# Optimization experiments

Hardware: AMD Instinct MI355X
Metric: run time of the kernel (lower is better)

## Reference

```python
import jax, jax.numpy as jnp
import numpy as np

HEADS = 16
DIM_HEAD = 64
NEG_INF = -1e30


def _rope_cos_sin(seq_len, dim_head, dtype):
    inv_freq = 1.0 / (10000.0 ** (jnp.arange(0, dim_head, 2, dtype=jnp.float32) / dim_head))
    t = jnp.arange(seq_len, dtype=jnp.float32)
    freqs = jnp.einsum('i,j->ij', t, inv_freq)          # [n, dh/2]
    emb = jnp.concatenate([freqs, freqs], axis=-1)       # [n, dh]
    return jnp.cos(emb).astype(dtype), jnp.sin(emb).astype(dtype)


def _rotate_half(x):
    x1, x2 = jnp.split(x, 2, axis=-1)
    return jnp.concatenate([-x2, x1], axis=-1)


def setup_inputs() -> dict:
    key = jax.random.key(0)
    k1, k2, k3 = jax.random.split(key, 3)
    dim = HEADS * DIM_HEAD  # 1024
    x = jax.random.normal(k1, (2, 2048, dim), dtype=jnp.float32)
    w_qkv = jax.random.normal(k2, (dim, 3 * dim), dtype=jnp.float32) * (dim ** -0.5)
    w_out = jax.random.normal(k3, (dim, dim), dtype=jnp.float32) * (dim ** -0.5)
    return {"x": x, "w_qkv": w_qkv, "w_out": w_out}


def reference(x, w_qkv, w_out):
    b, n, d = x.shape
    h, dh = HEADS, DIM_HEAD
    scale = dh ** -0.5

    qkv = x @ w_qkv                                      # [b, n, 3*h*dh]
    q, k, v = jnp.split(qkv, 3, axis=-1)
    reshape = lambda t: t.reshape(b, n, h, dh).transpose(0, 2, 1, 3)  # b h n dh
    q, k, v = reshape(q), reshape(k), reshape(v)

    cos, sin = _rope_cos_sin(n, dh, x.dtype)
    cos = cos[None, None, :, :]
    sin = sin[None, None, :, :]
    q = q * cos + _rotate_half(q) * sin
    k = k * cos + _rotate_half(k) * sin

    scores = jnp.einsum('bhid,bhjd->bhij', q, k) * scale  # [b, h, n, n]
    causal = jnp.triu(jnp.ones((n, n), dtype=bool), k=1)
    scores = jnp.where(causal[None, None, :, :], NEG_INF, scores)
    attn = jax.nn.softmax(scores, axis=-1)

    out = jnp.einsum('bhij,bhjd->bhid', attn, v)          # [b, h, n, dh]
    out = out.transpose(0, 2, 1, 3).reshape(b, n, h * dh)
    return out @ w_out
```

## Files before the change

### kernel.cpp

```cpp
#include <hip/hip_runtime.h>

#define SEQ 2048
#define NH 16
#define DH 64
#define DMODEL 1024
#define NQKV 3072

typedef __attribute__((ext_vector_type(8))) short bf16x8;
typedef __attribute__((ext_vector_type(4))) short bf16x4;
typedef __attribute__((ext_vector_type(4))) float f32x4;

#define GLOAD16(src, dst)                                                              \
  __builtin_amdgcn_global_load_lds((const __attribute__((address_space(1))) void*)(src), \
                                   (__attribute__((address_space(3))) void*)(dst), 16, 0, 0)

#define EXP2(x) __builtin_amdgcn_exp2f(x)

__device__ __forceinline__ unsigned short f2bf(float f) {
  union { float f; unsigned u; } v; v.f = f;
  unsigned r = v.u + 0x7FFFu + ((v.u >> 16) & 1u);
  return (unsigned short)(r >> 16);
}

__device__ __forceinline__ unsigned pkbf(float a, float b) {
  unsigned r;
  asm("v_cvt_pk_bf16_f32 %0, %1, %2" : "=v"(r) : "v"(a), "v"(b));
  return r;
}

__device__ __forceinline__ void transw_body(const float* __restrict__ in,
                                            unsigned short* __restrict__ out,
                                            int K, int N, int k0, int n0, int tid,
                                            float (*Ts)[65]) {
#pragma unroll
  for (int p = 0; p < 4; ++p) {
    int id = p * 256 + tid;
    int r = id >> 4, c4 = (id & 15) * 4;
    const f32x4 v = *reinterpret_cast<const f32x4*>(&in[(size_t)(k0 + r) * N + n0 + c4]);
    Ts[r][c4] = v[0]; Ts[r][c4 + 1] = v[1]; Ts[r][c4 + 2] = v[2]; Ts[r][c4 + 3] = v[3];
  }
  __syncthreads();
#pragma unroll
  for (int p = 0; p < 2; ++p) {
    int id = p * 256 + tid;
    int n = id >> 3, k8 = (id & 7) * 8;
    unsigned short tmp[8];
#pragma unroll
    for (int i = 0; i < 8; ++i) tmp[i] = f2bf(Ts[k8 + i][n]);
    *reinterpret_cast<bf16x8*>(&out[(size_t)(n0 + n) * K + k0 + k8]) =
        *reinterpret_cast<bf16x8*>(tmp);
  }
}

__global__ __launch_bounds__(256) void prep_kernel(
    const float* __restrict__ x, const float* __restrict__ w_qkv,
    const float* __restrict__ w_out, unsigned short* __restrict__ Xb,
    unsigned short* __restrict__ WqkvT, unsigned short* __restrict__ WoutT,
    float* __restrict__ cost, float* __restrict__ sint) {
  __shared__ float Ts[64][65];
  const int tid = threadIdx.x;
  const int id = blockIdx.x;
  if (id < 2048) {
    int idx = id * 256 + tid;
    const f32x4 v0 = *reinterpret_cast<const f32x4*>(&x[(size_t)idx * 8]);
    const f32x4 v1 = *reinterpret_cast<const f32x4*>(&x[(size_t)idx * 8 + 4]);
    bf16x8 o;
    o[0] = (short)f2bf(v0[0]); o[1] = (short)f2bf(v0[1]);
    o[2] = (short)f2bf(v0[2]); o[3] = (short)f2bf(v0[3]);
    o[4] = (short)f2bf(v1[0]); o[5] = (short)f2bf(v1[1]);
    o[6] = (short)f2bf(v1[2]); o[7] = (short)f2bf(v1[3]);
    *reinterpret_cast<bf16x8*>(&Xb[(size_t)idx * 8]) = o;
  } else if (id < 2816) {
    int t = id - 2048;
    transw_body(w_qkv, WqkvT, DMODEL, NQKV, (t & 15) * 64, (t >> 4) * 64, tid, Ts);
  } else if (id < 3072) {
    int t = id - 2816;
    transw_body(w_out, WoutT, DMODEL, DMODEL, (t & 15) * 64, (t >> 4) * 64, tid, Ts);
  } else {
    int idx = (id - 3072) * 256 + tid;
    int t = idx >> 5, j = idx & 31;
    float inv = powf(10000.0f, -(float)(2 * j) / 64.0f);
    float a = (float)t * inv;
    cost[idx] = cosf(a);
    sint[idx] = sinf(a);
  }
}

__global__ __launch_bounds__(256) void gemm_qkv_kernel(
    const unsigned short* __restrict__ Xb, const unsigned short* __restrict__ BT,
    unsigned short* __restrict__ Qb, unsigned short* __restrict__ Kb,
    unsigned short* __restrict__ Vtg,
    const float* __restrict__ cost, const float* __restrict__ sint) {
  __shared__ unsigned short As[2][8192];
  __shared__ unsigned short Bs[2][8192];

  const int tid = threadIdx.x;
  const int lane = tid & 63;
  const int w = tid >> 6;
  const int lam = lane & 15;
  const int g = lane >> 4;
  const int wr = w >> 1, wc = w & 1;
  const int rowBase = blockIdx.x * 128;
  const int colBase = blockIdx.y * 128;

  f32x4 acc[4][4];
#pragma unroll
  for (int m = 0; m < 4; ++m)
#pragma unroll
    for (int n = 0; n < 4; ++n) acc[m][n] = (f32x4){0.f, 0.f, 0.f, 0.f};

#define GSTAGE(buf, kk0)                                                               \
  {                                                                                    \
    _Pragma("unroll") for (int c = 0; c < 4; ++c) {                                    \
      int ch = c * 256 + w * 64 + lane;                                                \
      int row = ch >> 3, q = ch & 7;                                                   \
      GLOAD16(Xb + (size_t)(rowBase + row) * DMODEL + (kk0) + ((q ^ (row & 7)) * 8),   \
              &As[buf][0] + (c * 256 + w * 64) * 8);                                   \
      GLOAD16(BT + (size_t)(colBase + row) * DMODEL + (kk0) + ((q ^ (row & 7)) * 8),   \
              &Bs[buf][0] + (c * 256 + w * 64) * 8);                                   \
    }                                                                                  \
  }

  GSTAGE(0, 0);

  for (int kb = 0; kb < 16; ++kb) {
    if (kb + 1 < 16) {
      GSTAGE((kb + 1) & 1, (kb + 1) * 64);
      asm volatile("s_waitcnt vmcnt(8)" ::: "memory");
    } else {
      asm volatile("s_waitcnt vmcnt(0)" ::: "memory");
    }
    __builtin_amdgcn_s_barrier();
    const int cb = kb & 1;
#pragma unroll
    for (int kh = 0; kh < 2; ++kh) {
      bf16x8 a[4], b[4];
#pragma unroll
      for (int m = 0; m < 4; ++m) {
        int row = wr * 64 + m * 16 + lam;
        a[m] = *reinterpret_cast<bf16x8*>(&As[cb][row * 64 + (((kh * 4 + g) ^ (row & 7)) * 8)]);
      }
#pragma unroll
      for (int n = 0; n < 4; ++n) {
        int row = wc * 64 + n * 16 + lam;
        b[n] = *reinterpret_cast<bf16x8*>(&Bs[cb][row * 64 + (((kh * 4 + g) ^ (row & 7)) * 8)]);
      }
      __builtin_amdgcn_s_setprio(1);
#pragma unroll
      for (int m = 0; m < 4; ++m)
#pragma unroll
        for (int n = 0; n < 4; ++n)
          acc[m][n] = __builtin_amdgcn_mfma_f32_16x16x32_bf16(a[m], b[n], acc[m][n], 0, 0, 0);
      __builtin_amdgcn_s_setprio(0);
    }
    asm volatile("s_waitcnt lgkmcnt(0)" ::: "memory");
    __builtin_amdgcn_s_barrier();
  }
#undef GSTAGE

  const int mat = blockIdx.y >> 3;
  if (mat < 2) {
    unsigned short* dst = mat ? Kb : Qb;
    const float sc = mat ? 1.0f : 0.125f * 1.4426950408889634f;
    const int h = ((colBase & 1023) + wc * 64) >> 6;
#pragma unroll
    for (int m = 0; m < 4; ++m) {
#pragma unroll
      for (int r = 0; r < 4; ++r) {
        int row = rowBase + wr * 64 + m * 16 + g * 4 + r;
        int bi = row >> 11, t = row & 2047;
        unsigned short* out = &dst[(size_t)((bi * NH + h) * SEQ + t) * DH];
#pragma unroll
        for (int n = 0; n < 2; ++n) {
          int j = n * 16 + lam;
          float c = cost[t * 32 + j], s = sint[t * 32 + j];
          float x0 = acc[m][n][r], x1 = acc[m][n + 2][r];
          out[j] = f2bf((x0 * c - x1 * s) * sc);
          out[j + 32] = f2bf((x1 * c + x0 * s) * sc);
        }
      }
    }
  } else {
    unsigned short (*Vbuf)[44] = reinterpret_cast<unsigned short(*)[44]>(&As[0][0]);
    const int b = rowBase >> 11, t0 = rowBase & 2047;
#pragma unroll
    for (int cc = 0; cc < 4; ++cc) {
      __syncthreads();
      if (wc == (cc >> 1)) {
        const int n0 = (cc & 1) * 2;
#pragma unroll
        for (int m = 0; m < 4; ++m)
#pragma unroll
          for (int r = 0; r < 4; ++r)
#pragma unroll
            for (int n2 = 0; n2 < 2; ++n2)
              Vbuf[wr * 64 + m * 16 + g * 4 + r][n2 * 16 + lam] = f2bf(acc[m][n0 + n2][r]);
      }
      __syncthreads();
      const int colq0 = colBase - 2048 + cc * 32;
#pragma unroll
      for (int p2 = 0; p2 < 2; ++p2) {
        int ch = p2 * 256 + tid;
        int d = ch & 31, tq = (ch >> 5) * 8;
        unsigned short tmp[8];
#pragma unroll
        for (int i = 0; i < 8; ++i) tmp[i] = Vbuf[tq + i][d];
        int col = colq0 + d;
        int h = col >> 6, dd = col & 63;
        *reinterpret_cast<bf16x8*>(&Vtg[((size_t)(b * NH + h) * DH + dd) * SEQ + t0 + tq]) =
            *reinterpret_cast<bf16x8*>(tmp);
      }
    }
  }
}

__global__ __launch_bounds__(256) void attn_kernel(
    const unsigned short* __restrict__ Qb, const unsigned short* __restrict__ Kb,
    const unsigned short* __restrict__ Vtg, unsigned short* __restrict__ Ob) {
  __shared__ unsigned short Ks[2][8192];
  __shared__ unsigned short Vs[2][8192];
  __shared__ unsigned short Ps[4][2048];

  const int tid = threadIdx.x;
  const int lane = tid & 63;
  const int w = tid >> 6;
  const int lam = lane & 15;
  const int g = lane >> 4;
  const int bh = blockIdx.x;
  const int p = blockIdx.y;
  const int qtA = p, qtB = 31 - p;
  const int nA = (p >> 1) + 1;
  const int nB = ((31 - p) >> 1) + 1;
  const int nT = nA + nB;
  const int ql = w * 16 + lam;

  const unsigned short* kallbase = Kb + (size_t)bh * SEQ * DH;
  const unsigned short* vallbase = Vtg + (size_t)bh * DH * SEQ;

  bf16x8 qb0, qb1;
  f32x4 oacc[4], sa0[4], sa1[4];
  float mr, lr;

#define LOADQ(qt)                                                                     \
  {                                                                                   \
    const unsigned short* qrow = Qb + ((size_t)bh * SEQ + (qt) * 64 + w * 16 + lam) * DH; \
    qb0 = *reinterpret_cast<const bf16x8*>(&qrow[g * 8]);                             \
    qb1 = *reinterpret_cast<const bf16x8*>(&qrow[g * 8 + 32]);                        \
  }
#define RESET_STATE()                                                                 \
  {                                                                                   \
    _Pragma("unroll") for (int f = 0; f < 4; ++f) oacc[f] = (f32x4){0.f, 0.f, 0.f, 0.f}; \
    mr = -1e30f; lr = 0.f;                                                            \
  }
#define STAGE(buf, jt)                                                                \
  {                                                                                   \
    const unsigned short* kb2 = kallbase + (size_t)(jt) * 128 * DH;                   \
    const unsigned short* vb2 = vallbase + (size_t)(jt) * 128;                        \
    _Pragma("unroll") for (int c = 0; c < 4; ++c) {                                   \
      int id = c * 256 + w * 64 + lane;                                               \
      int kr = id >> 3, kq = id & 7;                                                  \
      GLOAD16(kb2 + kr * DH + ((kq ^ (kr & 7)) * 8), &Ks[buf][0] + id * 8);           \
      int vr = id >> 4, vq = id & 15;                                                 \
      GLOAD16(vb2 + (size_t)vr * SEQ + ((vq ^ (vr & 15)) * 8), &Vs[buf][0] + id * 8); \
    }                                                                                 \
  }
#define FLUSHO(qt)                                                                    \
  {                                                                                   \
    const int b = bh >> 4, h = bh & 15;                                               \
    float rinv = 1.0f / lr;                                                           \
    _Pragma("unroll") for (int r = 0; r < 4; ++r) {                                   \
      int n = (qt) * 64 + w * 16 + g * 4 + r;                                         \
      float inv = __shfl(rinv, g * 4 + r);                                            \
      unsigned short* orow = &Ob[(size_t)(b * SEQ + n) * DMODEL + h * DH];            \
      _Pragma("unroll") for (int f = 0; f < 4; ++f) orow[f * 16 + lam] = f2bf(oacc[f][r] * inv); \
    }                                                                                 \
  }

  RESET_STATE();
  LOADQ(qtA);
  STAGE(0, 0);
  asm volatile("s_waitcnt vmcnt(0)" ::: "memory");
  __syncthreads();

  int cur = 0;
  for (int i = 0; i < nT; ++i) {
    const int onA = (i < nA);
    const int qt = onA ? qtA : qtB;
    const int j = onA ? i : (i - nA);

    if (i + 1 < nT) {
      const int jn = (i + 1 < nA) ? (i + 1) : (i + 1 - nA);
      STAGE(cur ^ 1, jn);
    }

    const int t1 = 2 * j + 1;
    const bool diag0 = (2 * j == qt);
    const bool diag1 = (t1 == qt);
    const bool skip1 = (t1 > qt);

#pragma unroll
    for (int f = 0; f < 4; ++f) {
      sa0[f] = (f32x4){0.f, 0.f, 0.f, 0.f};
      sa1[f] = (f32x4){0.f, 0.f, 0.f, 0.f};
    }
    __builtin_amdgcn_s_setprio(1);
#pragma unroll
    for (int f = 0; f < 4; ++f) {
      int kr = f * 16 + lam;
      bf16x8 k0 = *reinterpret_cast<bf16x8*>(&Ks[cur][kr * 64 + ((g ^ (kr & 7)) * 8)]);
      bf16x8 k1 = *reinterpret_cast<bf16x8*>(&Ks[cur][kr * 64 + (((g + 4) ^ (kr & 7)) * 8)]);
      sa0[f] = __builtin_amdgcn_mfma_f32_16x16x32_bf16(k0, qb0, sa0[f], 0, 0, 0);
      sa0[f] = __builtin_amdgcn_mfma_f32_16x16x32_bf16(k1, qb1, sa0[f], 0, 0, 0);
    }
    if (!skip1) {
#pragma unroll
      for (int f = 0; f < 4; ++f) {
        int kr = 64 + f * 16 + lam;
        bf16x8 k0 = *reinterpret_cast<bf16x8*>(&Ks[cur][kr * 64 + ((g ^ (kr & 7)) * 8)]);
        bf16x8 k1 = *reinterpret_cast<bf16x8*>(&Ks[cur][kr * 64 + (((g + 4) ^ (kr & 7)) * 8)]);
        sa1[f] = __builtin_amdgcn_mfma_f32_16x16x32_bf16(k0, qb0, sa1[f], 0, 0, 0);
        sa1[f] = __builtin_amdgcn_mfma_f32_16x16x32_bf16(k1, qb1, sa1[f], 0, 0, 0);
      }
    }
    __builtin_amdgcn_s_setprio(0);

    if (diag0) {
#pragma unroll
      for (int f = 0; f < 4; ++f)
#pragma unroll
        for (int r = 0; r < 4; ++r)
          if (f * 16 + g * 4 + r > ql) sa0[f][r] = -1e30f;
    }
    if (diag1) {
#pragma unroll
      for (int f = 0; f < 4; ++f)
#pragma unroll
        for (int r = 0; r < 4; ++r)
          if (f * 16 + g * 4 + r > ql) sa1[f][r] = -1e30f;
    }

    float mx = -1e30f;
#pragma unroll
    for (int f = 0; f < 4; ++f)
#pragma unroll
      for (int r = 0; r < 4; ++r) mx = fmaxf(mx, sa0[f][r]);
    if (!skip1) {
#pragma unroll
      for (int f = 0; f < 4; ++f)
#pragma unroll
        for (int r = 0; r < 4; ++r) mx = fmaxf(mx, sa1[f][r]);
    }
    mx = fmaxf(mx, __shfl_xor(mx, 16));
    mx = fmaxf(mx, __shfl_xor(mx, 32));

    float mn = mr, alpha = 1.0f;
    if (!__all(mx - mr <= 8.0f)) {
      mn = fmaxf(mr, mx);
      alpha = EXP2(mr - mn);
      mr = mn;
#pragma unroll
      for (int r = 0; r < 4; ++r) {
        float af = __shfl(alpha, g * 4 + r);
#pragma unroll
        for (int f = 0; f < 4; ++f) oacc[f][r] *= af;
      }
    }

    float sum = 0.f;
#pragma unroll
    for (int f = 0; f < 4; ++f)
#pragma unroll
      for (int r = 0; r < 4; ++r) {
        sa0[f][r] = EXP2(sa0[f][r] - mn);
        sum += sa0[f][r];
      }
    if (!skip1) {
#pragma unroll
      for (int f = 0; f < 4; ++f)
#pragma unroll
        for (int r = 0; r < 4; ++r) {
          sa1[f][r] = EXP2(sa1[f][r] - mn);
          sum += sa1[f][r];
        }
    }
    sum += __shfl_xor(sum, 16);
    sum += __shfl_xor(sum, 32);
    lr = lr * alpha + sum;

#pragma unroll
    for (int f = 0; f < 4; ++f) {
      uint2 u;
      u.x = pkbf(sa0[f][0], sa0[f][1]);
      u.y = pkbf(sa0[f][2], sa0[f][3]);
      int chunk = f * 2 + (g >> 1);
      *reinterpret_cast<uint2*>(
          &Ps[w][lam * 128 + ((chunk ^ (lam & 15)) * 8) + ((g & 1) * 4)]) = u;
    }
    if (!skip1) {
#pragma unroll
      for (int f = 0; f < 4; ++f) {
        uint2 u;
        u.x = pkbf(sa1[f][0], sa1[f][1]);
        u.y = pkbf(sa1[f][2], sa1[f][3]);
        int chunk = 8 + f * 2 + (g >> 1);
        *reinterpret_cast<uint2*>(
            &Ps[w][lam * 128 + ((chunk ^ (lam & 15)) * 8) + ((g & 1) * 4)]) = u;
      }
    }

    bf16x8 pa0 = *reinterpret_cast<bf16x8*>(&Ps[w][lam * 128 + ((g ^ (lam & 15)) * 8)]);
    bf16x8 pa1 = *reinterpret_cast<bf16x8*>(&Ps[w][lam * 128 + (((4 + g) ^ (lam & 15)) * 8)]);
    __builtin_amdgcn_s_setprio(1);
#pragma unroll
    for (int f = 0; f < 4; ++f) {
      int vr = f * 16 + lam;
      bf16x8 v0 = *reinterpret_cast<bf16x8*>(&Vs[cur][vr * 128 + ((g ^ (vr & 15)) * 8)]);
      bf16x8 v1 = *reinterpret_cast<bf16x8*>(&Vs[cur][vr * 128 + (((4 + g) ^ (vr & 15)) * 8)]);
      oacc[f] = __builtin_amdgcn_mfma_f32_16x16x32_bf16(pa0, v0, oacc[f], 0, 0, 0);
      oacc[f] = __builtin_amdgcn_mfma_f32_16x16x32_bf16(pa1, v1, oacc[f], 0, 0, 0);
    }
    __builtin_amdgcn_s_setprio(0);
    if (!skip1) {
      bf16x8 pa2 = *reinterpret_cast<bf16x8*>(&Ps[w][lam * 128 + (((8 + g) ^ (lam & 15)) * 8)]);
      bf16x8 pa3 = *reinterpret_cast<bf16x8*>(&Ps[w][lam * 128 + (((12 + g) ^ (lam & 15)) * 8)]);
      __builtin_amdgcn_s_setprio(1);
#pragma unroll
      for (int f = 0; f < 4; ++f) {
        int vr = f * 16 + lam;
        bf16x8 v2 = *reinterpret_cast<bf16x8*>(&Vs[cur][vr * 128 + (((8 + g) ^ (vr & 15)) * 8)]);
        bf16x8 v3 = *reinterpret_cast<bf16x8*>(&Vs[cur][vr * 128 + (((12 + g) ^ (vr & 15)) * 8)]);
        oacc[f] = __builtin_amdgcn_mfma_f32_16x16x32_bf16(pa2, v2, oacc[f], 0, 0, 0);
        oacc[f] = __builtin_amdgcn_mfma_f32_16x16x32_bf16(pa3, v3, oacc[f], 0, 0, 0);
      }
      __builtin_amdgcn_s_setprio(0);
    }

    if (i == nA - 1) {
      FLUSHO(qtA);
      RESET_STATE();
      LOADQ(qtB);
    }

    asm volatile("s_waitcnt vmcnt(0)" ::: "memory");
    __syncthreads();
    cur ^= 1;
  }
  FLUSHO(qtB);
#undef LOADQ
#undef RESET_STATE
#undef STAGE
#undef FLUSHO
}

__global__ __launch_bounds__(256) void gemm_out_kernel(
    const unsigned short* __restrict__ A, const unsigned short* __restrict__ BT,
    float* __restrict__ C) {
  __shared__ unsigned short As[2][8192];
  __shared__ unsigned short Bs[2][8192];

  const int tid = threadIdx.x;
  const int lane = tid & 63;
  const int w = tid >> 6;
  const int lam = lane & 15;
  const int g = lane >> 4;
  const int wr = w >> 1, wc = w & 1;
  const int rowBase = blockIdx.x * 128;
  const int colBase = blockIdx.y * 128;

  f32x4 acc[4][4];
#pragma unroll
  for (int m = 0; m < 4; ++m)
#pragma unroll
    for (int n = 0; n < 4; ++n) acc[m][n] = (f32x4){0.f, 0.f, 0.f, 0.f};

#define GSTAGE(buf, kk0)                                                               \
  {                                                                                    \
    _Pragma("unroll") for (int c = 0; c < 4; ++c) {                                    \
      int ch = c * 256 + w * 64 + lane;                                                \
      int row = ch >> 3, q = ch & 7;                                                   \
      GLOAD16(A + (size_t)(rowBase + row) * DMODEL + (kk0) + ((q ^ (row & 7)) * 8),    \
              &As[buf][0] + (c * 256 + w * 64) * 8);                                   \
      GLOAD16(BT + (size_t)(colBase + row) * DMODEL + (kk0) + ((q ^ (row & 7)) * 8),   \
              &Bs[buf][0] + (c * 256 + w * 64) * 8);                                   \
    }                                                                                  \
  }

  GSTAGE(0, 0);

  for (int kb = 0; kb < 16; ++kb) {
    if (kb + 1 < 16) {
      GSTAGE((kb + 1) & 1, (kb + 1) * 64);
      asm volatile("s_waitcnt vmcnt(8)" ::: "memory");
    } else {
      asm volatile("s_waitcnt vmcnt(0)" ::: "memory");
    }
    __builtin_amdgcn_s_barrier();
    const int cb = kb & 1;
#pragma unroll
    for (int kh = 0; kh < 2; ++kh) {
      bf16x8 a[4], b[4];
#pragma unroll
      for (int m = 0; m < 4; ++m) {
        int row = wr * 64 + m * 16 + lam;
        a[m] = *reinterpret_cast<bf16x8*>(&As[cb][row * 64 + (((kh * 4 + g) ^ (row & 7)) * 8)]);
      }
#pragma unroll
      for (int n = 0; n < 4; ++n) {
        int row = wc * 64 + n * 16 + lam;
        b[n] = *reinterpret_cast<bf16x8*>(&Bs[cb][row * 64 + (((kh * 4 + g) ^ (row & 7)) * 8)]);
      }
      __builtin_amdgcn_s_setprio(1);
#pragma unroll
      for (int m = 0; m < 4; ++m)
#pragma unroll
        for (int n = 0; n < 4; ++n)
          acc[m][n] = __builtin_amdgcn_mfma_f32_16x16x32_bf16(a[m], b[n], acc[m][n], 0, 0, 0);
      __builtin_amdgcn_s_setprio(0);
    }
    asm volatile("s_waitcnt lgkmcnt(0)" ::: "memory");
    __builtin_amdgcn_s_barrier();
  }
#undef GSTAGE

#pragma unroll
  for (int m = 0; m < 4; ++m)
#pragma unroll
    for (int r = 0; r < 4; ++r) {
      int row = rowBase + wr * 64 + m * 16 + g * 4 + r;
#pragma unroll
      for (int n = 0; n < 4; ++n)
        C[(size_t)row * DMODEL + colBase + wc * 64 + n * 16 + lam] = acc[m][n][r];
    }
}

extern "C" void kernel_launch(void* const* d_in, const int* in_sizes, int n_in,
                              void* d_out, int out_size, void* d_ws, size_t ws_size,
                              hipStream_t stream) {
  const float* x = (const float*)d_in[0];
  const float* w_qkv = (const float*)d_in[1];
  const float* w_out = (const float*)d_in[2];
  float* out = (float*)d_out;

  char* ws = (char*)d_ws;
  const size_t MB = 1024 * 1024;
  unsigned short* WqkvT = (unsigned short*)(ws);
  float* cost = (float*)(ws + 6 * MB);
  float* sint = cost + SEQ * 32;
  unsigned short* Ob = (unsigned short*)(ws);
  unsigned short* WoutT = (unsigned short*)(ws + 8 * MB);
  unsigned short* Qb = (unsigned short*)(ws + 10 * MB);
  unsigned short* Kb = (unsigned short*)(ws + 18 * MB);
  unsigned short* Vtg = (unsigned short*)(ws + 26 * MB);
  unsigned short* Xb = (unsigned short*)d_out;

  prep_kernel<<<3328, 256, 0, stream>>>(x, w_qkv, w_out, Xb, WqkvT, WoutT, cost, sint);
  gemm_qkv_kernel<<<dim3(32, 24), 256, 0, stream>>>(Xb, WqkvT, Qb, Kb, Vtg, cost, sint);
  attn_kernel<<<dim3(32, 16), 256, 0, stream>>>(Qb, Kb, Vtg, Ob);
  gemm_out_kernel<<<dim3(32, 8), 256, 0, stream>>>(Ob, WoutT, out);
}
```

Measured before the change: 116.0 us.

## Single-buffer A tile in QKV GEMM with split-phase prefetch to cut LDS

```diff
diff --git a/kernel.cpp b/kernel.cpp
--- a/kernel.cpp
+++ b/kernel.cpp
@@ -91,7 +91,7 @@
     unsigned short* __restrict__ Qb, unsigned short* __restrict__ Kb,
     unsigned short* __restrict__ Vtg,
     const float* __restrict__ cost, const float* __restrict__ sint) {
-  __shared__ unsigned short As[2][8192];
+  __shared__ unsigned short As[8192];
   __shared__ unsigned short Bs[2][8192];
 
   const int tid = threadIdx.x;
@@ -109,54 +109,81 @@
 #pragma unroll
     for (int n = 0; n < 4; ++n) acc[m][n] = (f32x4){0.f, 0.f, 0.f, 0.f};
 
-#define GSTAGE(buf, kk0)                                                               \
+#define STAGE_A(kk0)                                                                   \
   {                                                                                    \
     _Pragma("unroll") for (int c = 0; c < 4; ++c) {                                    \
       int ch = c * 256 + w * 64 + lane;                                                \
       int row = ch >> 3, q = ch & 7;                                                   \
       GLOAD16(Xb + (size_t)(rowBase + row) * DMODEL + (kk0) + ((q ^ (row & 7)) * 8),   \
-              &As[buf][0] + (c * 256 + w * 64) * 8);                                   \
+              &As[0] + (c * 256 + w * 64) * 8);                                        \
+    }                                                                                  \
+  }
+#define STAGE_B(buf, kk0)                                                              \
+  {                                                                                    \
+    _Pragma("unroll") for (int c = 0; c < 4; ++c) {                                    \
+      int ch = c * 256 + w * 64 + lane;                                                \
+      int row = ch >> 3, q = ch & 7;                                                   \
       GLOAD16(BT + (size_t)(colBase + row) * DMODEL + (kk0) + ((q ^ (row & 7)) * 8),   \
               &Bs[buf][0] + (c * 256 + w * 64) * 8);                                   \
     }                                                                                  \
   }
 
-  GSTAGE(0, 0);
-
+  STAGE_A(0);
+  STAGE_B(0, 0);
+
+  int cur = 0;
   for (int kb = 0; kb < 16; ++kb) {
-    if (kb + 1 < 16) {
-      GSTAGE((kb + 1) & 1, (kb + 1) * 64);
-      asm volatile("s_waitcnt vmcnt(8)" ::: "memory");
-    } else {
-      asm volatile("s_waitcnt vmcnt(0)" ::: "memory");
-    }
+    asm volatile("s_waitcnt vmcnt(0)" ::: "memory");
     __builtin_amdgcn_s_barrier();
-    const int cb = kb & 1;
-#pragma unroll
-    for (int kh = 0; kh < 2; ++kh) {
-      bf16x8 a[4], b[4];
-#pragma unroll
-      for (int m = 0; m < 4; ++m) {
-        int row = wr * 64 + m * 16 + lam;
-        a[m] = *reinterpret_cast<bf16x8*>(&As[cb][row * 64 + (((kh * 4 + g) ^ (row & 7)) * 8)]);
-      }
-#pragma unroll
-      for (int n = 0; n < 4; ++n) {
-        int row = wc * 64 + n * 16 + lam;
-        b[n] = *reinterpret_cast<bf16x8*>(&Bs[cb][row * 64 + (((kh * 4 + g) ^ (row & 7)) * 8)]);
-      }
-      __builtin_amdgcn_s_setprio(1);
-#pragma unroll
-      for (int m = 0; m < 4; ++m)
-#pragma unroll
-        for (int n = 0; n < 4; ++n)
-          acc[m][n] = __builtin_amdgcn_mfma_f32_16x16x32_bf16(a[m], b[n], acc[m][n], 0, 0, 0);
-      __builtin_amdgcn_s_setprio(0);
+
+    if (kb + 1 < 16) STAGE_B(cur ^ 1, (kb + 1) * 64);
+
+    bf16x8 a[4], b[4];
+#pragma unroll
+    for (int m = 0; m < 4; ++m) {
+      int row = wr * 64 + m * 16 + lam;
+      a[m] = *reinterpret_cast<bf16x8*>(&As[row * 64 + ((g ^ (row & 7)) * 8)]);
+    }
+#pragma unroll
+    for (int n = 0; n < 4; ++n) {
+      int row = wc * 64 + n * 16 + lam;
+      b[n] = *reinterpret_cast<bf16x8*>(&Bs[cur][row * 64 + ((g ^ (row & 7)) * 8)]);
+    }
+    __builtin_amdgcn_s_setprio(1);
+#pragma unroll
+    for (int m = 0; m < 4; ++m)
+#pragma unroll
+      for (int n = 0; n < 4; ++n)
+        acc[m][n] = __builtin_amdgcn_mfma_f32_16x16x32_bf16(a[m], b[n], acc[m][n], 0, 0, 0);
+    __builtin_amdgcn_s_setprio(0);
+
+    bf16x8 a2[4], b2[4];
+#pragma unroll
+    for (int m = 0; m < 4; ++m) {
+      int row = wr * 64 + m * 16 + lam;
+      a2[m] = *reinterpret_cast<bf16x8*>(&As[row * 64 + (((4 + g) ^ (row & 7)) * 8)]);
+    }
+#pragma unroll
+    for (int n = 0; n < 4; ++n) {
+      int row = wc * 64 + n * 16 + lam;
+      b2[n] = *reinterpret_cast<bf16x8*>(&Bs[cur][row * 64 + (((4 + g) ^ (row & 7)) * 8)]);
     }
     asm volatile("s_waitcnt lgkmcnt(0)" ::: "memory");
     __builtin_amdgcn_s_barrier();
-  }
-#undef GSTAGE
+
+    if (kb + 1 < 16) STAGE_A((kb + 1) * 64);
+
+    __builtin_amdgcn_s_setprio(1);
+#pragma unroll
+    for (int m = 0; m < 4; ++m)
+#pragma unroll
+      for (int n = 0; n < 4; ++n)
+        acc[m][n] = __builtin_amdgcn_mfma_f32_16x16x32_bf16(a2[m], b2[n], acc[m][n], 0, 0, 0);
+    __builtin_amdgcn_s_setprio(0);
+    cur ^= 1;
+  }
+#undef STAGE_A
+#undef STAGE_B
 
   const int mat = blockIdx.y >> 3;
   if (mat < 2) {
@@ -181,7 +208,7 @@
       }
     }
   } else {
-    unsigned short (*Vbuf)[44] = reinterpret_cast<unsigned short(*)[44]>(&As[0][0]);
+    unsigned short (*Vbuf)[44] = reinterpret_cast<unsigned short(*)[44]>(&As[0]);
     const int b = rowBase >> 11, t0 = rowBase & 2047;
 #pragma unroll
     for (int cc = 0; cc < 4; ++cc) {
```

New measurement: 121.2 us. 1.05x slower.
